# Kernel optimization log

Measured on AMD Instinct MI355X. Metric: run time of the kernel, lower is better.

## Reference

```python
import jax, jax.numpy as jnp
import numpy as np

STRIDE = 1
PAD = 1

def setup_inputs() -> dict:
    key = jax.random.key(0)
    k1, k2 = jax.random.split(key)
    x = jax.random.normal(k1, (32, 128, 56, 56), dtype=jnp.float32)
    weight = jax.random.normal(k2, (256, 128, 3, 3), dtype=jnp.float32) * 0.1
    b = jnp.zeros((256,), dtype=jnp.float32)
    return {"x": x, "weight": weight, "b": b}

def reference(x, weight, b):
    # Binarize weights with sign (matches torch.sign: sign(0)=0), then plain conv2d.
    bw = jnp.sign(weight)
    out = jax.lax.conv_general_dilated(
        x, bw,
        window_strides=(STRIDE, STRIDE),
        padding=((PAD, PAD), (PAD, PAD)),
        dimension_numbers=("NCHW", "OIHW", "NCHW"),
    )
    return out + b[None, :, None, None]
```

## Files before the change

kernel.cpp:

```cpp
#include <hip/hip_runtime.h>
#include <hip/hip_bf16.h>

typedef __attribute__((ext_vector_type(8))) short bf16x8;
typedef __attribute__((ext_vector_type(4))) float f32x4;

#define CIN   128
#define COUT  256
#define NIMG  32
#define HWDIM 56
#define HPAD  58
#define KTOT  1152
#define HWIMG 3136
#define MTOT  100352
#define BS    128
#define BF    128
#define BK    64

__device__ __forceinline__ void gload16(const void* g, void* l) {
  __builtin_amdgcn_global_load_lds((const __attribute__((address_space(1))) void*)g,
                                   (__attribute__((address_space(3))) void*)l,
                                   16, 0, 0);
}

__global__ __launch_bounds__(256)
void zero_xp(float4* __restrict__ p, int n16) {
  int i = blockIdx.x * 256 + threadIdx.x;
  int stride = gridDim.x * 256;
  float4 z; z.x = 0.f; z.y = 0.f; z.z = 0.f; z.w = 0.f;
  for (; i < n16; i += stride) p[i] = z;
}

__global__ __launch_bounds__(256)
void prep_x(const float* __restrict__ x, __hip_bfloat16* __restrict__ xp) {
  __shared__ float tile[CIN * 57];
  const int nh = blockIdx.x;
  const int n = nh / HWDIM;
  const int h = nh - n * HWDIM;
  const int t = threadIdx.x;

  const float* src = x + (size_t)n * CIN * HWIMG + (size_t)h * HWDIM;
  for (int i = t; i < CIN * HWDIM; i += 256) {
    int c = i / HWDIM;
    int w = i - c * HWDIM;
    tile[c * 57 + w] = src[(size_t)c * HWIMG + w];
  }
  __syncthreads();

  __hip_bfloat16* dst = xp + (((size_t)n * HPAD + (h + 1)) * HPAD + 1) * CIN;
  for (int o = t; o < HWDIM * 64; o += 256) {
    int w = o >> 6;
    int c = (o & 63) * 2;
    __hip_bfloat162 pr;
    pr.x = __float2bfloat16(tile[c * 57 + w]);
    pr.y = __float2bfloat16(tile[(c + 1) * 57 + w]);
    *reinterpret_cast<__hip_bfloat162*>(dst + (size_t)w * CIN + c) = pr;
  }
}

__global__ __launch_bounds__(256)
void prep_w(const float* __restrict__ wsrc, __hip_bfloat16* __restrict__ wt) {
  int o = blockIdx.x * 256 + threadIdx.x;
  if (o >= COUT * KTOT) return;
  int cout = o / KTOT;
  int r = o - cout * KTOT;
  int tap = r >> 7;
  int cin = r & 127;
  float v = wsrc[((size_t)cout * CIN + cin) * 9 + tap];
  float s = (v > 0.f) ? 1.f : ((v < 0.f) ? -1.f : 0.f);
  wt[o] = __float2bfloat16(s);
}

__global__ __launch_bounds__(256, 2)
void bconv_mfma(const short* __restrict__ xp, const short* __restrict__ wt,
                const float* __restrict__ bias, float* __restrict__ out) {
  __shared__ short lw[BF * BK];
  __shared__ short lx[BS * BK];

  const int tid  = threadIdx.x;
  const int lane = tid & 63;
  const int wv   = tid >> 6;
  const int wm   = wv >> 1;
  const int wn   = wv & 1;
  const int s0   = blockIdx.x * BS;
  const int f0   = blockIdx.y * BF;

  const int srow = tid >> 3;
  const int slot = tid & 7;
  const int swz  = slot ^ (srow & 7);

  int xoff[4];
  int woff[4];
#pragma unroll
  for (int r = 0; r < 4; ++r) {
    int m  = s0 + r * 32 + srow;
    int n  = m / HWIMG;
    int hw = m - n * HWIMG;
    int h  = hw / HWDIM;
    int w  = hw - h * HWDIM;
    xoff[r] = ((n * HPAD + h) * HPAD + w) * CIN + swz * 8;
    woff[r] = (f0 + r * 32 + srow) * KTOT + swz * 8;
  }

  f32x4 acc[4][4] = {};

  short* lwdst = &lw[(wv * 8) * BK];
  short* lxdst = &lx[(wv * 8) * BK];

  for (int ks = 0; ks < 18; ++ks) {
    const int tap = ks >> 1;
    const int kh  = tap / 3;
    const int kw  = tap - kh * 3;
    const int xko = (kh * HPAD + kw) * CIN + (ks & 1) * BK;
    const int wko = ks * BK;

    __syncthreads();
#pragma unroll
    for (int r = 0; r < 4; ++r) {
      gload16(wt + woff[r] + wko, lwdst + r * 32 * BK);
      gload16(xp + xoff[r] + xko, lxdst + r * 32 * BK);
    }
    __syncthreads();

#pragma unroll
    for (int ksub = 0; ksub < 2; ++ksub) {
      const int rlo = lane & 15;
      const int sx  = (ksub * 4 + (lane >> 4)) ^ (rlo & 7);
      bf16x8 af[4], bx[4];
#pragma unroll
      for (int f = 0; f < 4; ++f) {
        int row = wm * 64 + f * 16 + rlo;
        af[f] = *(const bf16x8*)&lw[row * BK + sx * 8];
      }
#pragma unroll
      for (int f = 0; f < 4; ++f) {
        int row = wn * 64 + f * 16 + rlo;
        bx[f] = *(const bf16x8*)&lx[row * BK + sx * 8];
      }
#pragma unroll
      for (int fm = 0; fm < 4; ++fm)
#pragma unroll
        for (int fn = 0; fn < 4; ++fn)
          acc[fm][fn] = __builtin_amdgcn_mfma_f32_16x16x32_bf16(
              af[fm], bx[fn], acc[fm][fn], 0, 0, 0);
    }
  }

  const int col = lane & 15;
  const int rg  = lane >> 4;
#pragma unroll
  for (int fn = 0; fn < 4; ++fn) {
    int m  = s0 + wn * 64 + fn * 16 + col;
    int n  = m / HWIMG;
    int hw = m - n * HWIMG;
    float* obase = out + (size_t)n * (COUT * HWIMG) + hw;
#pragma unroll
    for (int fm = 0; fm < 4; ++fm) {
      int c0 = f0 + wm * 64 + fm * 16 + rg * 4;
#pragma unroll
      for (int j = 0; j < 4; ++j) {
        int c = c0 + j;
        obase[(size_t)c * HWIMG] = acc[fm][fn][j] + bias[c];
      }
    }
  }
}

extern "C" void kernel_launch(void* const* d_in, const int* in_sizes, int n_in,
                              void* d_out, int out_size, void* d_ws, size_t ws_size,
                              hipStream_t stream) {
  const float* x  = (const float*)d_in[0];
  const float* w  = (const float*)d_in[1];
  const float* b  = (const float*)d_in[2];
  float* out = (float*)d_out;

  const size_t xp_elems = (size_t)NIMG * HPAD * HPAD * CIN;
  __hip_bfloat16* xp = (__hip_bfloat16*)d_ws;
  __hip_bfloat16* wt = xp + xp_elems;

  int n16 = (int)(xp_elems / 8);
  zero_xp<<<2048, 256, 0, stream>>>((float4*)d_ws, n16);

  prep_x<<<NIMG * HWDIM, 256, 0, stream>>>(x, xp);

  prep_w<<<(COUT * KTOT + 255) / 256, 256, 0, stream>>>(w, wt);

  dim3 grid(MTOT / BS, COUT / BF);
  bconv_mfma<<<grid, 256, 0, stream>>>((const short*)xp, (const short*)wt, b, out);
}
```

Baseline: 103.4 us.

## Fuse prep kernels, remap block order, swap MFMA operands for vector stores

Result: faster. 89.15 us (-13.8%).

```diff
diff --git a/kernel.cpp b/kernel.cpp
--- a/kernel.cpp
+++ b/kernel.cpp
@@ -12,9 +12,8 @@
 #define KTOT  1152
 #define HWIMG 3136
 #define MTOT  100352
-#define BS    128
-#define BF    128
 #define BK    64
+#define NT    18
 
 __device__ __forceinline__ void gload16(const void* g, void* l) {
   __builtin_amdgcn_global_load_lds((const __attribute__((address_space(1))) void*)g,
@@ -23,66 +22,68 @@
 }
 
 __global__ __launch_bounds__(256)
-void zero_xp(float4* __restrict__ p, int n16) {
-  int i = blockIdx.x * 256 + threadIdx.x;
-  int stride = gridDim.x * 256;
-  float4 z; z.x = 0.f; z.y = 0.f; z.z = 0.f; z.w = 0.f;
-  for (; i < n16; i += stride) p[i] = z;
-}
-
-__global__ __launch_bounds__(256)
-void prep_x(const float* __restrict__ x, __hip_bfloat16* __restrict__ xp) {
+void prep_all(const float* __restrict__ x, const float* __restrict__ w,
+              __hip_bfloat16* __restrict__ xp, __hip_bfloat16* __restrict__ wt) {
   __shared__ float tile[CIN * 57];
-  const int nh = blockIdx.x;
-  const int n = nh / HWDIM;
-  const int h = nh - n * HWDIM;
+  const int bid = blockIdx.x;
   const int t = threadIdx.x;
-
-  const float* src = x + (size_t)n * CIN * HWIMG + (size_t)h * HWDIM;
-  for (int i = t; i < CIN * HWDIM; i += 256) {
-    int c = i / HWDIM;
-    int w = i - c * HWDIM;
-    tile[c * 57 + w] = src[(size_t)c * HWIMG + w];
-  }
-  __syncthreads();
-
-  __hip_bfloat16* dst = xp + (((size_t)n * HPAD + (h + 1)) * HPAD + 1) * CIN;
-  for (int o = t; o < HWDIM * 64; o += 256) {
-    int w = o >> 6;
-    int c = (o & 63) * 2;
-    __hip_bfloat162 pr;
-    pr.x = __float2bfloat16(tile[c * 57 + w]);
-    pr.y = __float2bfloat16(tile[(c + 1) * 57 + w]);
-    *reinterpret_cast<__hip_bfloat162*>(dst + (size_t)w * CIN + c) = pr;
+  if (bid < NIMG * HPAD) {
+    const int n = bid / HPAD;
+    const int h = bid - n * HPAD;
+    __hip_bfloat16* dstrow = xp + ((size_t)n * HPAD + h) * HPAD * CIN;
+    int4 z; z.x = 0; z.y = 0; z.z = 0; z.w = 0;
+    if (h == 0 || h == HPAD - 1) {
+      for (int i = t; i < (HPAD * CIN) / 8; i += 256)
+        reinterpret_cast<int4*>(dstrow)[i] = z;
+      return;
+    }
+    const float* src = x + (size_t)n * CIN * HWIMG + (size_t)(h - 1) * HWDIM;
+    for (int i = t; i < CIN * HWDIM; i += 256) {
+      int c = i / HWDIM;
+      int wd = i - c * HWDIM;
+      tile[c * 57 + wd] = src[(size_t)c * HWIMG + wd];
+    }
+    if (t < 32) {
+      int side = t >> 4;
+      reinterpret_cast<int4*>(dstrow + (side ? (HPAD - 1) : 0) * CIN)[t & 15] = z;
+    }
+    __syncthreads();
+    __hip_bfloat16* dst = dstrow + CIN;
+    for (int o = t; o < HWDIM * 64; o += 256) {
+      int wd = o >> 6;
+      int c = (o & 63) * 2;
+      __hip_bfloat162 pr;
+      pr.x = __float2bfloat16(tile[c * 57 + wd]);
+      pr.y = __float2bfloat16(tile[(c + 1) * 57 + wd]);
+      *reinterpret_cast<__hip_bfloat162*>(dst + (size_t)wd * CIN + c) = pr;
+    }
+  } else {
+    int o = (bid - NIMG * HPAD) * 256 + t;
+    int cout = o / KTOT;
+    int r = o - cout * KTOT;
+    int tap = r >> 7;
+    int cin = r & 127;
+    float v = w[((size_t)cout * CIN + cin) * 9 + tap];
+    wt[o] = __float2bfloat16(v > 0.f ? 1.f : (v < 0.f ? -1.f : 0.f));
   }
 }
 
-__global__ __launch_bounds__(256)
-void prep_w(const float* __restrict__ wsrc, __hip_bfloat16* __restrict__ wt) {
-  int o = blockIdx.x * 256 + threadIdx.x;
-  if (o >= COUT * KTOT) return;
-  int cout = o / KTOT;
-  int r = o - cout * KTOT;
-  int tap = r >> 7;
-  int cin = r & 127;
-  float v = wsrc[((size_t)cout * CIN + cin) * 9 + tap];
-  float s = (v > 0.f) ? 1.f : ((v < 0.f) ? -1.f : 0.f);
-  wt[o] = __float2bfloat16(s);
-}
-
-__global__ __launch_bounds__(256, 2)
-void bconv_mfma(const short* __restrict__ xp, const short* __restrict__ wt,
-                const float* __restrict__ bias, float* __restrict__ out) {
-  __shared__ short lw[BF * BK];
-  __shared__ short lx[BS * BK];
+__global__ __launch_bounds__(256, 4)
+void bconv(const short* __restrict__ xp, const short* __restrict__ wt,
+           const float* __restrict__ bias, float* __restrict__ out) {
+  __shared__ short lw[128 * BK];
+  __shared__ short lx[128 * BK];
 
   const int tid  = threadIdx.x;
   const int lane = tid & 63;
   const int wv   = tid >> 6;
   const int wm   = wv >> 1;
   const int wn   = wv & 1;
-  const int s0   = blockIdx.x * BS;
-  const int f0   = blockIdx.y * BF;
+
+  const int myid = blockIdx.y * 784 + blockIdx.x;
+  const int sid  = (myid & 7) * 196 + (myid >> 3);
+  const int s0   = (sid >> 1) * 128;
+  const int f0   = (sid & 1) * 128;
 
   const int srow = tid >> 3;
   const int slot = tid & 7;
@@ -106,7 +107,7 @@
   short* lwdst = &lw[(wv * 8) * BK];
   short* lxdst = &lx[(wv * 8) * BK];
 
-  for (int ks = 0; ks < 18; ++ks) {
+  for (int ks = 0; ks < NT; ++ks) {
     const int tap = ks >> 1;
     const int kh  = tap / 3;
     const int kw  = tap - kh * 3;
@@ -121,46 +122,48 @@
     }
     __syncthreads();
 
+    const int rlo = lane & 15;
 #pragma unroll
     for (int ksub = 0; ksub < 2; ++ksub) {
-      const int rlo = lane & 15;
-      const int sx  = (ksub * 4 + (lane >> 4)) ^ (rlo & 7);
+      const int sx = (ksub * 4 + (lane >> 4)) ^ (rlo & 7);
       bf16x8 af[4], bx[4];
 #pragma unroll
-      for (int f = 0; f < 4; ++f) {
-        int row = wm * 64 + f * 16 + rlo;
-        af[f] = *(const bf16x8*)&lw[row * BK + sx * 8];
-      }
+      for (int f = 0; f < 4; ++f)
+        af[f] = *(const bf16x8*)&lw[(wm * 64 + f * 16 + rlo) * BK + sx * 8];
 #pragma unroll
-      for (int f = 0; f < 4; ++f) {
-        int row = wn * 64 + f * 16 + rlo;
-        bx[f] = *(const bf16x8*)&lx[row * BK + sx * 8];
-      }
+      for (int f = 0; f < 4; ++f)
+        bx[f] = *(const bf16x8*)&lx[(wn * 64 + f * 16 + rlo) * BK + sx * 8];
 #pragma unroll
       for (int fm = 0; fm < 4; ++fm)
 #pragma unroll
         for (int fn = 0; fn < 4; ++fn)
           acc[fm][fn] = __builtin_amdgcn_mfma_f32_16x16x32_bf16(
-              af[fm], bx[fn], acc[fm][fn], 0, 0, 0);
+              bx[fn], af[fm], acc[fm][fn], 0, 0, 0);
     }
   }
 
   const int col = lane & 15;
   const int rg  = lane >> 4;
+  int nb[4], hwb[4];
 #pragma unroll
   for (int fn = 0; fn < 4; ++fn) {
-    int m  = s0 + wn * 64 + fn * 16 + col;
-    int n  = m / HWIMG;
-    int hw = m - n * HWIMG;
-    float* obase = out + (size_t)n * (COUT * HWIMG) + hw;
+    int m16 = s0 + wn * 64 + fn * 16;
+    int n = m16 / HWIMG;
+    nb[fn]  = n;
+    hwb[fn] = m16 - n * HWIMG + rg * 4;
+  }
 #pragma unroll
-    for (int fm = 0; fm < 4; ++fm) {
-      int c0 = f0 + wm * 64 + fm * 16 + rg * 4;
+  for (int fm = 0; fm < 4; ++fm) {
+    int cc = f0 + wm * 64 + fm * 16 + col;
+    float bv = bias[cc];
 #pragma unroll
-      for (int j = 0; j < 4; ++j) {
-        int c = c0 + j;
-        obase[(size_t)c * HWIMG] = acc[fm][fn][j] + bias[c];
-      }
+    for (int fn = 0; fn < 4; ++fn) {
+      float4 v;
+      v.x = acc[fm][fn][0] + bv;
+      v.y = acc[fm][fn][1] + bv;
+      v.z = acc[fm][fn][2] + bv;
+      v.w = acc[fm][fn][3] + bv;
+      *reinterpret_cast<float4*>(out + ((size_t)nb[fn] * COUT + cc) * HWIMG + hwb[fn]) = v;
     }
   }
 }
@@ -168,22 +171,17 @@
 extern "C" void kernel_launch(void* const* d_in, const int* in_sizes, int n_in,
                               void* d_out, int out_size, void* d_ws, size_t ws_size,
                               hipStream_t stream) {
-  const float* x  = (const float*)d_in[0];
-  const float* w  = (const float*)d_in[1];
-  const float* b  = (const float*)d_in[2];
+  const float* x = (const float*)d_in[0];
+  const float* w = (const float*)d_in[1];
+  const float* b = (const float*)d_in[2];
   float* out = (float*)d_out;
 
   const size_t xp_elems = (size_t)NIMG * HPAD * HPAD * CIN;
   __hip_bfloat16* xp = (__hip_bfloat16*)d_ws;
   __hip_bfloat16* wt = xp + xp_elems;
 
-  int n16 = (int)(xp_elems / 8);
-  zero_xp<<<2048, 256, 0, stream>>>((float4*)d_ws, n16);
+  prep_all<<<NIMG * HPAD + (COUT * KTOT) / 256, 256, 0, stream>>>(x, w, xp, wt);
 
-  prep_x<<<NIMG * HWDIM, 256, 0, stream>>>(x, xp);
-
-  prep_w<<<(COUT * KTOT + 255) / 256, 256, 0, stream>>>(w, wt);
-
-  dim3 grid(MTOT / BS, COUT / BF);
-  bconv_mfma<<<grid, 256, 0, stream>>>((const short*)xp, (const short*)wt, b, out);
+  dim3 grid(MTOT / 128, COUT / 128);
+  bconv<<<grid, 256, 0, stream>>>((const short*)xp, (const short*)wt, b, out);
 }
```
